# Kernel optimization log

Measured on AMD Instinct MI355X. Metric: run time of the kernel, lower is better.

The kernel has to match this reference:

```python
import jax, jax.numpy as jnp
import numpy as np

HIDDEN = 1024
NUM_HEADS = 16
HEAD_SIZE = HIDDEN // NUM_HEADS


def setup_inputs() -> dict:
    key = jax.random.key(0)
    ks = jax.random.split(key, 5)
    B, S = 2, 2048
    x = jax.random.normal(ks[0], (B, S, HIDDEN), dtype=jnp.float32)
    # nn.Linear(hidden, 3*hidden): weight stored (in, out) for x @ W
    scale_qkv = 1.0 / np.sqrt(HIDDEN)
    w_qkv = jax.random.uniform(ks[1], (HIDDEN, 3 * HIDDEN), minval=-scale_qkv, maxval=scale_qkv, dtype=jnp.float32)
    b_qkv = jax.random.uniform(ks[2], (3 * HIDDEN,), minval=-scale_qkv, maxval=scale_qkv, dtype=jnp.float32)
    w_o = jax.random.uniform(ks[3], (HIDDEN, HIDDEN), minval=-scale_qkv, maxval=scale_qkv, dtype=jnp.float32)
    b_o = jax.random.uniform(ks[4], (HIDDEN,), minval=-scale_qkv, maxval=scale_qkv, dtype=jnp.float32)
    return {"x": x, "w_qkv": w_qkv, "b_qkv": b_qkv, "w_o": w_o, "b_o": b_o}


def reference(x, w_qkv, b_qkv, w_o, b_o):
    B, S, H = x.shape
    qkv = x @ w_qkv + b_qkv  # (B, S, 3H)
    q, k, v = jnp.split(qkv, 3, axis=-1)
    # (B, S, H) -> (B, nheads, S, head_size)
    def heads(t):
        return t.reshape(B, S, NUM_HEADS, HEAD_SIZE).transpose(0, 2, 1, 3)
    q, k, v = heads(q), heads(k), heads(v)
    scores = jnp.einsum('bhqd,bhkd->bhqk', q, k) / np.sqrt(HEAD_SIZE).astype(np.float32)
    causal = jnp.tril(jnp.ones((S, S), dtype=bool))  # k <= q
    scores = jnp.where(causal, scores, -jnp.inf)
    probs = jax.nn.softmax(scores, axis=-1)
    out = jnp.einsum('bhqk,bhkd->bqhd', probs, v).reshape(B, S, H)
    return out @ w_o + b_o
```

## Files before the change

### kernel.cpp

```cpp
#include <hip/hip_runtime.h>
#include <stdint.h>


typedef __bf16 bf16;
typedef __attribute__((ext_vector_type(8))) __bf16 bf16x8;
typedef __attribute__((ext_vector_type(4))) __bf16 bf16x4;
typedef __attribute__((ext_vector_type(4))) float floatx4;

#define SCL 0.18033688011112042f

__device__ __forceinline__ floatx4 mfma_bf16(bf16x8 a, bf16x8 b, floatx4 c) {
  return __builtin_amdgcn_mfma_f32_16x16x32_bf16(a, b, c, 0, 0, 0);
}

__device__ __forceinline__ void cp_g2l_16(const bf16* g, bf16* l) {
  __builtin_amdgcn_global_load_lds(
      (const __attribute__((address_space(1))) void*)g,
      (__attribute__((address_space(3))) void*)l, 16, 0, 0);
}

__global__ __launch_bounds__(256) void prep_kernel(
    const float* __restrict__ x, bf16* __restrict__ xb,
    const float* __restrict__ w_qkv, bf16* __restrict__ wqkvt,
    const float* __restrict__ w_o, bf16* __restrict__ wot) {
  const int b = blockIdx.x;
  const int tid = threadIdx.x;
  if (b < 4096) {
    const int i = (b * 256 + tid) * 4;
    floatx4 v = *(const floatx4*)(x + i);
    bf16x4 o;
    o[0] = (bf16)v[0]; o[1] = (bf16)v[1]; o[2] = (bf16)v[2]; o[3] = (bf16)v[3];
    *(bf16x4*)(xb + i) = o;
    return;
  }
  __shared__ float tile[32][33];
  const float* W; bf16* Wt; int K, N, n0, k0;
  if (b < 7168) {
    const int bb = b - 4096;
    W = w_qkv; Wt = wqkvt; K = 1024; N = 3072;
    n0 = (bb % 96) * 32; k0 = (bb / 96) * 32;
  } else {
    const int bb = b - 7168;
    W = w_o; Wt = wot; K = 1024; N = 1024;
    n0 = (bb & 31) * 32; k0 = (bb >> 5) * 32;
  }
  const int tx = tid & 31, ty = tid >> 5;
  for (int i = 0; i < 4; ++i)
    tile[ty + 8 * i][tx] = W[(size_t)(k0 + ty + 8 * i) * N + n0 + tx];
  __syncthreads();
  for (int i = 0; i < 4; ++i)
    Wt[(size_t)(n0 + ty + 8 * i) * K + k0 + tx] = (bf16)tile[tx][ty + 8 * i];
}

template <int MODE, int MI>
__global__ __launch_bounds__(256, 3) void gemm_bt_kernel(
    const bf16* __restrict__ A, const bf16* __restrict__ Bt,
    const float* __restrict__ bias, float* __restrict__ outF,
    bf16* __restrict__ qb, bf16* __restrict__ kb, bf16* __restrict__ vtb,
    int N, int K) {
  constexpr int BM = MI * 32;
  __shared__ bf16 As[BM * 32];
  __shared__ bf16 Bs[128 * 32];
  const int tid = threadIdx.x;
  const int w = tid >> 6, lane = tid & 63;
  const int l16 = lane & 15, quad = lane >> 4;
  const int m0 = blockIdx.y * BM, n0 = blockIdx.x * 128;
  const int wm = (w & 1) * (BM / 2), wn = (w >> 1) * 64;

  const int arow = w * (BM / 4) + (lane >> 2);
  const int acol = (lane & 3) * 8;
  const bf16* Ag = A + (size_t)(m0 + arow) * K + acol;
  bf16* Al = As + arow * 32 + acol;
  const int brow = w * 32 + (lane >> 2);
  const bf16* Bg = Bt + (size_t)(n0 + brow) * K + acol;
  bf16* Bl = Bs + brow * 32 + acol;

  floatx4 acc[MI][4];
#pragma unroll
  for (int i = 0; i < MI; ++i)
#pragma unroll
    for (int j = 0; j < 4; ++j) acc[i][j] = (floatx4){0.f, 0.f, 0.f, 0.f};

  for (int k0 = 0; k0 < K; k0 += 32) {
    __syncthreads();
    cp_g2l_16(Ag + k0, Al);
    if (MI == 4) cp_g2l_16(Ag + (size_t)16 * K + k0, Al + 16 * 32);
    cp_g2l_16(Bg + k0, Bl);
    cp_g2l_16(Bg + (size_t)16 * K + k0, Bl + 16 * 32);
    __syncthreads();
    bf16x8 af[MI], bfr[4];
#pragma unroll
    for (int i = 0; i < MI; ++i)
      af[i] = *(const bf16x8*)(&As[(wm + i * 16 + l16) * 32 + quad * 8]);
#pragma unroll
    for (int j = 0; j < 4; ++j)
      bfr[j] = *(const bf16x8*)(&Bs[(wn + j * 16 + l16) * 32 + quad * 8]);
#pragma unroll
    for (int i = 0; i < MI; ++i)
#pragma unroll
      for (int j = 0; j < 4; ++j)
        acc[i][j] = mfma_bf16(af[i], bfr[j], acc[i][j]);
  }

#pragma unroll
  for (int i = 0; i < MI; ++i)
#pragma unroll
    for (int j = 0; j < 4; ++j) {
      const int nn = n0 + wn + j * 16 + l16;
      const float bv = bias[nn];
      const int mbase = m0 + wm + i * 16 + quad * 4;
      if (MODE == 1) {
#pragma unroll
        for (int r = 0; r < 4; ++r)
          outF[(size_t)(mbase + r) * N + nn] = acc[i][j][r] + bv;
      } else {
        const int which = nn >> 10;
        const int rem = nn & 1023;
        const int h = rem >> 6, d = rem & 63;
        const int b = mbase >> 11, s = mbase & 2047;
        const size_t bh = (size_t)(b * 16 + h);
        if (which == 2) {
          bf16x4 pk;
#pragma unroll
          for (int r = 0; r < 4; ++r) pk[r] = (bf16)(acc[i][j][r] + bv);
          *(bf16x4*)(vtb + (bh * 64 + d) * 2048 + s) = pk;
        } else if (which == 0) {
#pragma unroll
          for (int r = 0; r < 4; ++r)
            qb[(bh * 2048 + s + r) * 64 + d] = (bf16)((acc[i][j][r] + bv) * SCL);
        } else {
#pragma unroll
          for (int r = 0; r < 4; ++r)
            kb[(bh * 2048 + s + r) * 64 + d] = (bf16)(acc[i][j][r] + bv);
        }
      }
    }
}

__global__ __launch_bounds__(256, 3) void attn_kernel(
    const bf16* __restrict__ Qb, const bf16* __restrict__ Kb,
    const bf16* __restrict__ Vtb, bf16* __restrict__ attnb) {
  __shared__ bf16 Ks[2][4096];
  __shared__ bf16 Vs[2][4096];
  __shared__ bf16 Ps[4 * 2368];
  const int bid = blockIdx.x;
  const int bh = (bid & 7) * 4 + ((bid >> 3) & 3);
  const int p = bid >> 5;
  const int tid = threadIdx.x;
  const int w = tid >> 6, lane = tid & 63;
  const int l16 = lane & 15, quad = lane >> 4;
  const int qt = (w < 2) ? p : (31 - p);
  const int q0 = qt * 64 + (w & 1) * 32;
  const int b = bh >> 4, h = bh & 15;
  const bf16* Qh = Qb + (size_t)bh * 2048 * 64;
  const bf16* Kh = Kb + (size_t)bh * 2048 * 64;
  const bf16* Vh = Vtb + (size_t)bh * 64 * 2048;
  bf16* Pw = Ps + w * 2368;
  const int pw_wr = quad * 288 + (quad >> 1) * 16 + l16;
  const int pw_rd = l16 * 72 + (l16 >> 3) * 16 + quad * 8;

  const int nt = 32 - p;
  const int wdiag = qt;

  const int c0 = tid, c1 = 256 + tid;
  const int ksrc0 = (c0 >> 3) * 64 + (((c0 & 7) - (c0 >> 3)) & 7) * 8;
  const int ksrc1 = (c1 >> 3) * 64 + (((c1 & 7) - (c1 >> 3)) & 7) * 8;
  const int vsrc0 = (c0 >> 3) * 2048 + (((c0 & 7) - (c0 >> 3)) & 7) * 8;
  const int vsrc1 = (c1 >> 3) * 2048 + (((c1 & 7) - (c1 >> 3)) & 7) * 8;

  bf16x8 qf[2][2];
#pragma unroll
  for (int mb = 0; mb < 2; ++mb)
#pragma unroll
    for (int kq = 0; kq < 2; ++kq)
      qf[mb][kq] = *(const bf16x8*)(Qh + (size_t)(q0 + mb * 16 + l16) * 64 +
                                    kq * 32 + quad * 8);
  bf16x8 ones;
#pragma unroll
  for (int j = 0; j < 8; ++j) ones[j] = (bf16)1.0f;

  floatx4 O[2][4], Ol[2];
#pragma unroll
  for (int mb = 0; mb < 2; ++mb) {
#pragma unroll
    for (int nd = 0; nd < 4; ++nd) O[mb][nd] = (floatx4){0.f, 0.f, 0.f, 0.f};
    Ol[mb] = (floatx4){0.f, 0.f, 0.f, 0.f};
  }

  cp_g2l_16(Kh + ksrc0, &Ks[0][c0 * 8]);
  cp_g2l_16(Kh + ksrc1, &Ks[0][c1 * 8]);
  cp_g2l_16(Vh + vsrc0, &Vs[0][c0 * 8]);
  cp_g2l_16(Vh + vsrc1, &Vs[0][c1 * 8]);

  int cur = 0;
  for (int t = 0; t < nt; ++t, cur ^= 1) {
    __syncthreads();
    if (t + 1 < nt) {
      const bf16* KtG = Kh + (size_t)(t + 1) * 4096;
      const bf16* VtG = Vh + (t + 1) * 64;
      const int nb = cur ^ 1;
      cp_g2l_16(KtG + ksrc0, &Ks[nb][c0 * 8]);
      cp_g2l_16(KtG + ksrc1, &Ks[nb][c1 * 8]);
      cp_g2l_16(VtG + vsrc0, &Vs[nb][c0 * 8]);
      cp_g2l_16(VtG + vsrc1, &Vs[nb][c1 * 8]);
    }

    if (t > wdiag) continue;
    const bool diag = (t == wdiag);
    const bf16* KsC = Ks[cur];
    const bf16* VsC = Vs[cur];

    bf16x8 kf[4][2];
#pragma unroll
    for (int nk = 0; nk < 4; ++nk)
#pragma unroll
      for (int kq = 0; kq < 2; ++kq) {
        const int row = nk * 16 + l16;
        kf[nk][kq] = *(const bf16x8*)(
            &KsC[row * 64 + ((kq * 4 + quad + row) & 7) * 8]);
      }

    {
      floatx4 sf[4];
#pragma unroll
      for (int nk = 0; nk < 4; ++nk) {
        floatx4 a = (floatx4){0.f, 0.f, 0.f, 0.f};
        a = mfma_bf16(qf[0][0], kf[nk][0], a);
        a = mfma_bf16(qf[0][1], kf[nk][1], a);
        sf[nk] = a;
      }
#pragma unroll
      for (int nk = 0; nk < 4; ++nk)
#pragma unroll
        for (int r = 0; r < 4; ++r) {
          float s = sf[nk][r];
          if (diag) {
            const int kc = t * 64 + nk * 16 + l16;
            const int qrow = q0 + quad * 4 + r;
            s = (kc <= qrow) ? s : -1e30f;
          }
          Pw[pw_wr + r * 72 + nk * 16] = (bf16)__builtin_amdgcn_exp2f(s);
        }
    }
    floatx4 sg[4];
#pragma unroll
    for (int nk = 0; nk < 4; ++nk) {
      floatx4 a = (floatx4){0.f, 0.f, 0.f, 0.f};
      a = mfma_bf16(qf[1][0], kf[nk][0], a);
      a = mfma_bf16(qf[1][1], kf[nk][1], a);
      sg[nk] = a;
    }
    bf16x8 vf[4][2];
#pragma unroll
    for (int nd = 0; nd < 4; ++nd)
#pragma unroll
      for (int kq = 0; kq < 2; ++kq) {
        const int row = nd * 16 + l16;
        vf[nd][kq] = *(const bf16x8*)(
            &VsC[row * 64 + ((kq * 4 + quad + row) & 7) * 8]);
      }
#pragma unroll
    for (int nk = 0; nk < 4; ++nk)
#pragma unroll
      for (int r = 0; r < 4; ++r) {
        float s = sg[nk][r];
        if (diag) {
          const int kc = t * 64 + nk * 16 + l16;
          const int qrow = q0 + 16 + quad * 4 + r;
          s = (kc <= qrow) ? s : -1e30f;
        }
        Pw[pw_wr + 1184 + r * 72 + nk * 16] = (bf16)__builtin_amdgcn_exp2f(s);
      }

#pragma unroll
    for (int mb = 0; mb < 2; ++mb) {
      bf16x8 pf[2];
      pf[0] = *(const bf16x8*)(&Pw[pw_rd + mb * 1184]);
      pf[1] = *(const bf16x8*)(&Pw[pw_rd + mb * 1184 + 32]);
#pragma unroll
      for (int nd = 0; nd < 4; ++nd) {
        floatx4 o = O[mb][nd];
        o = mfma_bf16(pf[0], vf[nd][0], o);
        o = mfma_bf16(pf[1], vf[nd][1], o);
        O[mb][nd] = o;
      }
      Ol[mb] = mfma_bf16(pf[0], ones, Ol[mb]);
      Ol[mb] = mfma_bf16(pf[1], ones, Ol[mb]);
    }
  }

#pragma unroll
  for (int mb = 0; mb < 2; ++mb)
#pragma unroll
    for (int r = 0; r < 4; ++r) {
      const int qrow = q0 + mb * 16 + quad * 4 + r;
      const float inv = 1.f / Ol[mb][r];
#pragma unroll
      for (int nd = 0; nd < 4; ++nd)
        attnb[((size_t)(b * 2048 + qrow)) * 1024 + h * 64 + nd * 16 + l16] =
            (bf16)(O[mb][nd][r] * inv);
    }
}

extern "C" void kernel_launch(void* const* d_in, const int* in_sizes, int n_in,
                              void* d_out, int out_size, void* d_ws, size_t ws_size,
                              hipStream_t stream) {
  const float* x     = (const float*)d_in[0];
  const float* w_qkv = (const float*)d_in[1];
  const float* b_qkv = (const float*)d_in[2];
  const float* w_o   = (const float*)d_in[3];
  const float* b_o   = (const float*)d_in[4];
  float* out = (float*)d_out;

  char* ws = (char*)d_ws;
  bf16* xb    = (bf16*)ws; ws += (size_t)4096 * 1024 * 2;
  bf16* wqkvt = (bf16*)ws; ws += (size_t)3072 * 1024 * 2;
  bf16* wot   = (bf16*)ws; ws += (size_t)1024 * 1024 * 2;
  bf16* qb    = (bf16*)ws; ws += (size_t)32 * 2048 * 64 * 2;
  bf16* kb    = (bf16*)ws; ws += (size_t)32 * 2048 * 64 * 2;
  bf16* vtb   = (bf16*)ws; ws += (size_t)32 * 2048 * 64 * 2;
  bf16* attnb = (bf16*)ws; ws += (size_t)4096 * 1024 * 2;

  prep_kernel<<<8192, 256, 0, stream>>>(x, xb, w_qkv, wqkvt, w_o, wot);
  gemm_bt_kernel<0, 4><<<dim3(24, 32), 256, 0, stream>>>(
      xb, wqkvt, b_qkv, nullptr, qb, kb, vtb, 3072, 1024);
  attn_kernel<<<512, 256, 0, stream>>>(qb, kb, vtb, attnb);
  gemm_bt_kernel<1, 2><<<dim3(8, 64), 256, 0, stream>>>(
      attnb, wot, b_o, out, nullptr, nullptr, nullptr, 1024, 1024);
}
```

Measured before the change: 191.4 us.

## Use 512-thread attention blocks with 16 query rows per wave

The attention kernel now runs 8 waves per block, each owning 16 query rows instead of 32, with four waves on the low tile and four on the mirrored high tile. The QK^T product is computed transposed (K as the A operand), so each lane holds four consecutive keys and writes P to LDS as packed bf16x4 stores instead of scalar stores. Each thread now issues a single async K/V copy per tile. The aim is more waves to hide latency and cheaper P staging, at the cost of redoing the K/V fragment loads per 16 rows and more block-wide barrier participants.

```diff
diff --git a/kernel.cpp b/kernel.cpp
--- a/kernel.cpp
+++ b/kernel.cpp
@@ -137,72 +137,57 @@
     }
 }
 
-__global__ __launch_bounds__(256, 3) void attn_kernel(
+__global__ __launch_bounds__(512, 4) void attn_kernel(
     const bf16* __restrict__ Qb, const bf16* __restrict__ Kb,
     const bf16* __restrict__ Vtb, bf16* __restrict__ attnb) {
   __shared__ bf16 Ks[2][4096];
   __shared__ bf16 Vs[2][4096];
-  __shared__ bf16 Ps[4 * 2368];
+  __shared__ bf16 Ps[8 * 1152];
   const int bid = blockIdx.x;
   const int bh = (bid & 7) * 4 + ((bid >> 3) & 3);
   const int p = bid >> 5;
   const int tid = threadIdx.x;
   const int w = tid >> 6, lane = tid & 63;
   const int l16 = lane & 15, quad = lane >> 4;
-  const int qt = (w < 2) ? p : (31 - p);
-  const int q0 = qt * 64 + (w & 1) * 32;
+  const int g = (w < 4) ? p : (31 - p);
+  const int q0 = g * 64 + (w & 3) * 16;
   const int b = bh >> 4, h = bh & 15;
   const bf16* Qh = Qb + (size_t)bh * 2048 * 64;
   const bf16* Kh = Kb + (size_t)bh * 2048 * 64;
   const bf16* Vh = Vtb + (size_t)bh * 64 * 2048;
-  bf16* Pw = Ps + w * 2368;
-  const int pw_wr = quad * 288 + (quad >> 1) * 16 + l16;
-  const int pw_rd = l16 * 72 + (l16 >> 3) * 16 + quad * 8;
+  bf16* Pw = Ps + w * 1152;
 
   const int nt = 32 - p;
-  const int wdiag = qt;
-
-  const int c0 = tid, c1 = 256 + tid;
-  const int ksrc0 = (c0 >> 3) * 64 + (((c0 & 7) - (c0 >> 3)) & 7) * 8;
-  const int ksrc1 = (c1 >> 3) * 64 + (((c1 & 7) - (c1 >> 3)) & 7) * 8;
-  const int vsrc0 = (c0 >> 3) * 2048 + (((c0 & 7) - (c0 >> 3)) & 7) * 8;
-  const int vsrc1 = (c1 >> 3) * 2048 + (((c1 & 7) - (c1 >> 3)) & 7) * 8;
-
-  bf16x8 qf[2][2];
-#pragma unroll
-  for (int mb = 0; mb < 2; ++mb)
-#pragma unroll
-    for (int kq = 0; kq < 2; ++kq)
-      qf[mb][kq] = *(const bf16x8*)(Qh + (size_t)(q0 + mb * 16 + l16) * 64 +
-                                    kq * 32 + quad * 8);
+  const int wdiag = g;
+
+  const int srow = tid >> 3;
+  const int ssl = ((tid & 7) - srow) & 7;
+  const int ksrc = srow * 64 + ssl * 8;
+  const int vsrc = srow * 2048 + ssl * 8;
+
+  bf16x8 qf[2];
+#pragma unroll
+  for (int kq = 0; kq < 2; ++kq)
+    qf[kq] = *(const bf16x8*)(Qh + (size_t)(q0 + l16) * 64 + kq * 32 + quad * 8);
   bf16x8 ones;
 #pragma unroll
   for (int j = 0; j < 8; ++j) ones[j] = (bf16)1.0f;
 
-  floatx4 O[2][4], Ol[2];
-#pragma unroll
-  for (int mb = 0; mb < 2; ++mb) {
-#pragma unroll
-    for (int nd = 0; nd < 4; ++nd) O[mb][nd] = (floatx4){0.f, 0.f, 0.f, 0.f};
-    Ol[mb] = (floatx4){0.f, 0.f, 0.f, 0.f};
-  }
-
-  cp_g2l_16(Kh + ksrc0, &Ks[0][c0 * 8]);
-  cp_g2l_16(Kh + ksrc1, &Ks[0][c1 * 8]);
-  cp_g2l_16(Vh + vsrc0, &Vs[0][c0 * 8]);
-  cp_g2l_16(Vh + vsrc1, &Vs[0][c1 * 8]);
+  floatx4 O[4], Ol;
+#pragma unroll
+  for (int nd = 0; nd < 4; ++nd) O[nd] = (floatx4){0.f, 0.f, 0.f, 0.f};
+  Ol = (floatx4){0.f, 0.f, 0.f, 0.f};
+
+  cp_g2l_16(Kh + ksrc, &Ks[0][tid * 8]);
+  cp_g2l_16(Vh + vsrc, &Vs[0][tid * 8]);
 
   int cur = 0;
   for (int t = 0; t < nt; ++t, cur ^= 1) {
     __syncthreads();
     if (t + 1 < nt) {
-      const bf16* KtG = Kh + (size_t)(t + 1) * 4096;
-      const bf16* VtG = Vh + (t + 1) * 64;
       const int nb = cur ^ 1;
-      cp_g2l_16(KtG + ksrc0, &Ks[nb][c0 * 8]);
-      cp_g2l_16(KtG + ksrc1, &Ks[nb][c1 * 8]);
-      cp_g2l_16(VtG + vsrc0, &Vs[nb][c0 * 8]);
-      cp_g2l_16(VtG + vsrc1, &Vs[nb][c1 * 8]);
+      cp_g2l_16(Kh + (size_t)(t + 1) * 4096 + ksrc, &Ks[nb][tid * 8]);
+      cp_g2l_16(Vh + (t + 1) * 64 + vsrc, &Vs[nb][tid * 8]);
     }
 
     if (t > wdiag) continue;
@@ -220,36 +205,15 @@
             &KsC[row * 64 + ((kq * 4 + quad + row) & 7) * 8]);
       }
 
-    {
-      floatx4 sf[4];
-#pragma unroll
-      for (int nk = 0; nk < 4; ++nk) {
-        floatx4 a = (floatx4){0.f, 0.f, 0.f, 0.f};
-        a = mfma_bf16(qf[0][0], kf[nk][0], a);
-        a = mfma_bf16(qf[0][1], kf[nk][1], a);
-        sf[nk] = a;
-      }
-#pragma unroll
-      for (int nk = 0; nk < 4; ++nk)
-#pragma unroll
-        for (int r = 0; r < 4; ++r) {
-          float s = sf[nk][r];
-          if (diag) {
-            const int kc = t * 64 + nk * 16 + l16;
-            const int qrow = q0 + quad * 4 + r;
-            s = (kc <= qrow) ? s : -1e30f;
-          }
-          Pw[pw_wr + r * 72 + nk * 16] = (bf16)__builtin_amdgcn_exp2f(s);
-        }
-    }
-    floatx4 sg[4];
+    floatx4 sf[4];
 #pragma unroll
     for (int nk = 0; nk < 4; ++nk) {
       floatx4 a = (floatx4){0.f, 0.f, 0.f, 0.f};
-      a = mfma_bf16(qf[1][0], kf[nk][0], a);
-      a = mfma_bf16(qf[1][1], kf[nk][1], a);
-      sg[nk] = a;
-    }
+      a = mfma_bf16(kf[nk][0], qf[0], a);
+      a = mfma_bf16(kf[nk][1], qf[1], a);
+      sf[nk] = a;
+    }
+
     bf16x8 vf[4][2];
 #pragma unroll
     for (int nd = 0; nd < 4; ++nd)
@@ -259,47 +223,47 @@
         vf[nd][kq] = *(const bf16x8*)(
             &VsC[row * 64 + ((kq * 4 + quad + row) & 7) * 8]);
       }
-#pragma unroll
-    for (int nk = 0; nk < 4; ++nk)
+
+#pragma unroll
+    for (int nk = 0; nk < 4; ++nk) {
+      bf16x4 pk;
 #pragma unroll
       for (int r = 0; r < 4; ++r) {
-        float s = sg[nk][r];
+        float s = sf[nk][r];
         if (diag) {
-          const int kc = t * 64 + nk * 16 + l16;
-          const int qrow = q0 + 16 + quad * 4 + r;
+          const int kc = t * 64 + nk * 16 + quad * 4 + r;
+          const int qrow = q0 + l16;
           s = (kc <= qrow) ? s : -1e30f;
         }
-        Pw[pw_wr + 1184 + r * 72 + nk * 16] = (bf16)__builtin_amdgcn_exp2f(s);
-      }
-
-#pragma unroll
-    for (int mb = 0; mb < 2; ++mb) {
-      bf16x8 pf[2];
-      pf[0] = *(const bf16x8*)(&Pw[pw_rd + mb * 1184]);
-      pf[1] = *(const bf16x8*)(&Pw[pw_rd + mb * 1184 + 32]);
-#pragma unroll
-      for (int nd = 0; nd < 4; ++nd) {
-        floatx4 o = O[mb][nd];
-        o = mfma_bf16(pf[0], vf[nd][0], o);
-        o = mfma_bf16(pf[1], vf[nd][1], o);
-        O[mb][nd] = o;
-      }
-      Ol[mb] = mfma_bf16(pf[0], ones, Ol[mb]);
-      Ol[mb] = mfma_bf16(pf[1], ones, Ol[mb]);
-    }
-  }
-
-#pragma unroll
-  for (int mb = 0; mb < 2; ++mb)
-#pragma unroll
-    for (int r = 0; r < 4; ++r) {
-      const int qrow = q0 + mb * 16 + quad * 4 + r;
-      const float inv = 1.f / Ol[mb][r];
-#pragma unroll
-      for (int nd = 0; nd < 4; ++nd)
-        attnb[((size_t)(b * 2048 + qrow)) * 1024 + h * 64 + nd * 16 + l16] =
-            (bf16)(O[mb][nd][r] * inv);
-    }
+        pk[r] = (bf16)__builtin_amdgcn_exp2f(s);
+      }
+      *(bf16x4*)(&Pw[l16 * 72 + nk * 16 + quad * 4]) = pk;
+    }
+
+    bf16x8 pf[2];
+    pf[0] = *(const bf16x8*)(&Pw[l16 * 72 + quad * 8]);
+    pf[1] = *(const bf16x8*)(&Pw[l16 * 72 + 32 + quad * 8]);
+
+#pragma unroll
+    for (int nd = 0; nd < 4; ++nd) {
+      floatx4 o = O[nd];
+      o = mfma_bf16(pf[0], vf[nd][0], o);
+      o = mfma_bf16(pf[1], vf[nd][1], o);
+      O[nd] = o;
+    }
+    Ol = mfma_bf16(pf[0], ones, Ol);
+    Ol = mfma_bf16(pf[1], ones, Ol);
+  }
+
+#pragma unroll
+  for (int r = 0; r < 4; ++r) {
+    const int qrow = q0 + quad * 4 + r;
+    const float inv = 1.f / Ol[r];
+#pragma unroll
+    for (int nd = 0; nd < 4; ++nd)
+      attnb[((size_t)(b * 2048 + qrow)) * 1024 + h * 64 + nd * 16 + l16] =
+          (bf16)(O[nd][r] * inv);
+  }
 }
 
 extern "C" void kernel_launch(void* const* d_in, const int* in_sizes, int n_in,
@@ -324,7 +288,7 @@
   prep_kernel<<<8192, 256, 0, stream>>>(x, xb, w_qkv, wqkvt, w_o, wot);
   gemm_bt_kernel<0, 4><<<dim3(24, 32), 256, 0, stream>>>(
       xb, wqkvt, b_qkv, nullptr, qb, kb, vtb, 3072, 1024);
-  attn_kernel<<<512, 256, 0, stream>>>(qb, kb, vtb, attnb);
+  attn_kernel<<<512, 512, 0, stream>>>(qb, kb, vtb, attnb);
   gemm_bt_kernel<1, 2><<<dim3(8, 64), 256, 0, stream>>>(
       attnb, wot, b_o, out, nullptr, nullptr, nullptr, 1024, 1024);
 }
```

After: 175.9 us. 1.09x faster.
